# Performance work log

Hardware: AMD Instinct MI355X
Metric: run time of the kernel (lower is better)

Reference implementation:

```python
import jax, jax.numpy as jnp
import numpy as np

N_NODES = 50000
N_EDGES = 1_600_000
IN_FEATS = 256
N_HEADS = 2
OUT_FEATS = 64
NEG_SLOPE = 0.2


def setup_inputs() -> dict:
    key = jax.random.key(0)
    k1, k2, k3, k4, k5, k6 = jax.random.split(key, 6)
    feat = jax.random.normal(k1, (N_NODES, IN_FEATS), dtype=jnp.float32)
    src = jax.random.randint(k2, (N_EDGES,), 0, N_NODES, dtype=jnp.int32)
    dst = jax.random.randint(k3, (N_EDGES,), 0, N_NODES, dtype=jnp.int32)
    W = jax.random.normal(k4, (IN_FEATS, N_HEADS * OUT_FEATS), dtype=jnp.float32) * 0.05
    attn_l = jax.random.normal(k5, (N_HEADS, OUT_FEATS), dtype=jnp.float32) * 0.1
    attn_r = jax.random.normal(k6, (N_HEADS, OUT_FEATS), dtype=jnp.float32) * 0.1
    return {"feat": feat, "src": src, "dst": dst, "W": W, "attn_l": attn_l, "attn_r": attn_r}


def reference(feat, src, dst, W, attn_l, attn_r):
    # node projection: [N, H, F]
    ft = (feat @ W).reshape(N_NODES, N_HEADS, OUT_FEATS)
    el = jnp.einsum('nhf,hf->nh', ft, attn_l)  # [N, H]
    er = jnp.einsum('nhf,hf->nh', ft, attn_r)  # [N, H]
    # per-edge logits + leaky relu
    e = el[src] + er[dst]                      # [E, H]
    e = jnp.where(e > 0, e, NEG_SLOPE * e)
    # segment softmax over incoming edges of each dst node
    m = jax.ops.segment_max(e, dst, num_segments=N_NODES)     # [N, H]
    m = jnp.where(jnp.isfinite(m), m, 0.0)                     # guard empty segments
    e_exp = jnp.exp(e - jax.lax.stop_gradient(m)[dst])         # [E, H]
    s = jax.ops.segment_sum(e_exp, dst, num_segments=N_NODES)  # [N, H]
    a = e_exp / jnp.maximum(s[dst], 1e-20)                     # [E, H]
    # scatter-weighted aggregation: sum_e a_e * ft[src_e] into dst
    msg = ft[src] * a[:, :, None]                              # [E, H, F]
    rst = jax.ops.segment_sum(msg, dst, num_segments=N_NODES)  # [N, H, F]
    return rst
```

## Files before the change

### kernel.cpp

```cpp
#include <hip/hip_runtime.h>
#include <hip/hip_fp16.h>

#define N_NODES 50000
#define N_EDGES 1600000
#define IN_F 256
#define NEG_SLOPE 0.2f
#define CHUNK 1024
#define NCH ((N_NODES + CHUNK - 1) / CHUNK)

__global__ __launch_bounds__(256) void k_gemm(const float* __restrict__ feat,
                                              const float* __restrict__ W,
                                              const float* __restrict__ attn_l,
                                              const float* __restrict__ attn_r,
                                              __half* __restrict__ ft16,
                                              float* __restrict__ el,
                                              float* __restrict__ er) {
  __shared__ __align__(16) float Wl[32 * 128];
  __shared__ __align__(16) float Fl[64 * 33];
  const int tid = threadIdx.x;
  const int cg = tid & 15;
  const int rg = tid >> 4;
  const int col0 = cg * 8, rowt = rg * 4;
  const int row0 = blockIdx.x * 64;
  float acc[4][8];
#pragma unroll
  for (int i = 0; i < 4; ++i)
#pragma unroll
    for (int j = 0; j < 8; ++j) acc[i][j] = 0.f;

  for (int kt = 0; kt < IN_F; kt += 32) {
    __syncthreads();
#pragma unroll
    for (int j = 0; j < 4; ++j) {
      int idx = tid + j * 256;
      ((float4*)Wl)[idx] = ((const float4*)(W + kt * 128))[idx];
    }
#pragma unroll
    for (int j = 0; j < 2; ++j) {
      int r = j * 32 + (tid >> 3);
      int kk = (tid & 7) * 4;
      int grow = row0 + r;
      if (grow >= N_NODES) grow = N_NODES - 1;
      float4 v = *(const float4*)(feat + (size_t)grow * IN_F + kt + kk);
      float* fp = &Fl[r * 33 + kk];
      fp[0] = v.x; fp[1] = v.y; fp[2] = v.z; fp[3] = v.w;
    }
    __syncthreads();
#pragma unroll
    for (int k = 0; k < 32; ++k) {
      float4 w0 = *(const float4*)&Wl[k * 128 + col0];
      float4 w1 = *(const float4*)&Wl[k * 128 + col0 + 4];
#pragma unroll
      for (int i = 0; i < 4; ++i) {
        float f = Fl[(rowt + i) * 33 + k];
        acc[i][0] = fmaf(f, w0.x, acc[i][0]);
        acc[i][1] = fmaf(f, w0.y, acc[i][1]);
        acc[i][2] = fmaf(f, w0.z, acc[i][2]);
        acc[i][3] = fmaf(f, w0.w, acc[i][3]);
        acc[i][4] = fmaf(f, w1.x, acc[i][4]);
        acc[i][5] = fmaf(f, w1.y, acc[i][5]);
        acc[i][6] = fmaf(f, w1.z, acc[i][6]);
        acc[i][7] = fmaf(f, w1.w, acc[i][7]);
      }
    }
  }
  float al[8], ar[8];
#pragma unroll
  for (int j = 0; j < 8; ++j) { al[j] = attn_l[col0 + j]; ar[j] = attn_r[col0 + j]; }
#pragma unroll
  for (int i = 0; i < 4; ++i) {
    int row = row0 + rowt + i;
    float sl = 0.f, sr = 0.f;
#pragma unroll
    for (int j = 0; j < 8; ++j) { sl = fmaf(acc[i][j], al[j], sl); sr = fmaf(acc[i][j], ar[j], sr); }
#pragma unroll
    for (int m = 1; m < 8; m <<= 1) { sl += __shfl_xor(sl, m, 64); sr += __shfl_xor(sr, m, 64); }
    if (row < N_NODES) {
      __half2 h0 = __floats2half2_rn(acc[i][0], acc[i][1]);
      __half2 h1 = __floats2half2_rn(acc[i][2], acc[i][3]);
      __half2 h2 = __floats2half2_rn(acc[i][4], acc[i][5]);
      __half2 h3 = __floats2half2_rn(acc[i][6], acc[i][7]);
      uint4 pk = make_uint4(*(unsigned*)&h0, *(unsigned*)&h1,
                            *(unsigned*)&h2, *(unsigned*)&h3);
      *(uint4*)(ft16 + (size_t)row * 128 + col0) = pk;
      if ((cg & 7) == 0) {
        int h = cg >> 3;
        el[row * 2 + h] = sl;
        er[row * 2 + h] = sr;
      }
    }
  }
}

__global__ __launch_bounds__(256) void k_deg(const int* __restrict__ dst,
                                             int* __restrict__ deg,
                                             ushort* __restrict__ rank) {
  int t = blockIdx.x * 256 + threadIdx.x;
  if (t >= N_EDGES / 4) return;
  int4 d4 = ((const int4*)dst)[t];
  ushort4 r;
  r.x = (ushort)atomicAdd(&deg[d4.x], 1);
  r.y = (ushort)atomicAdd(&deg[d4.y], 1);
  r.z = (ushort)atomicAdd(&deg[d4.z], 1);
  r.w = (ushort)atomicAdd(&deg[d4.w], 1);
  ((ushort4*)rank)[t] = r;
}

__global__ __launch_bounds__(256) void k_scanA(const int* __restrict__ deg,
                                               int* __restrict__ csum) {
  __shared__ int ws[4];
  int b = blockIdx.x, tid = threadIdx.x, lane = tid & 63, w = tid >> 6;
  int i0 = b * CHUNK + tid * 4;
  int s = 0;
#pragma unroll
  for (int j = 0; j < 4; ++j) {
    int i = i0 + j;
    if (i < N_NODES) s += deg[i];
  }
#pragma unroll
  for (int m = 32; m > 0; m >>= 1) s += __shfl_xor(s, m, 64);
  if (lane == 0) ws[w] = s;
  __syncthreads();
  if (tid == 0) csum[b] = ws[0] + ws[1] + ws[2] + ws[3];
}

__global__ void k_scanB(const int* __restrict__ csum, int* __restrict__ coff,
                        int* __restrict__ rowptr) {
  int tid = threadIdx.x;
  int v = (tid < NCH) ? csum[tid] : 0;
  int x = v;
#pragma unroll
  for (int off = 1; off < 64; off <<= 1) {
    int y = __shfl_up(x, off, 64);
    if (tid >= off) x += y;
  }
  if (tid < NCH) coff[tid] = x - v;
  if (tid == NCH - 1) rowptr[N_NODES] = x;
}

__global__ __launch_bounds__(256) void k_scanC(const int* __restrict__ deg,
                                               const int* __restrict__ coff,
                                               int* __restrict__ rowptr) {
  __shared__ int wtot[4];
  int b = blockIdx.x, tid = threadIdx.x, lane = tid & 63, w = tid >> 6;
  int i0 = b * CHUNK + tid * 4;
  int d[4];
#pragma unroll
  for (int j = 0; j < 4; ++j) d[j] = (i0 + j < N_NODES) ? deg[i0 + j] : 0;
  int t1 = d[0] + d[1], t2 = t1 + d[2], t3 = t2 + d[3];
  int x = t3;
#pragma unroll
  for (int off = 1; off < 64; off <<= 1) {
    int y = __shfl_up(x, off, 64);
    if (lane >= off) x += y;
  }
  if (lane == 63) wtot[w] = x;
  __syncthreads();
  int woff = 0;
  for (int j = 0; j < w; ++j) woff += wtot[j];
  int excl = coff[b] + woff + (x - t3);
  int pre[4] = {0, d[0], t1, t2};
#pragma unroll
  for (int j = 0; j < 4; ++j) {
    int i = i0 + j;
    if (i < N_NODES) rowptr[i] = excl + pre[j];
  }
}

__global__ __launch_bounds__(256) void k_sort(const int* __restrict__ src,
                                              const int* __restrict__ dst,
                                              const ushort* __restrict__ rank,
                                              const int* __restrict__ rowptr,
                                              int* __restrict__ srcs) {
  int t = blockIdx.x * 256 + threadIdx.x;
  if (t >= N_EDGES / 4) return;
  int4 s4 = ((const int4*)src)[t];
  int4 d4 = ((const int4*)dst)[t];
  ushort4 r4 = ((const ushort4*)rank)[t];
  srcs[rowptr[d4.x] + r4.x] = s4.x;
  srcs[rowptr[d4.y] + r4.y] = s4.y;
  srcs[rowptr[d4.z] + r4.z] = s4.z;
  srcs[rowptr[d4.w] + r4.w] = s4.w;
}

__global__ __launch_bounds__(256) void k_agg(const int* __restrict__ srcs,
                                             const int* __restrict__ rowptr,
                                             const __half2* __restrict__ ft2,
                                             const float2* __restrict__ el2,
                                             const float2* __restrict__ er2,
                                             float2* __restrict__ out) {
  int t = blockIdx.x * 256 + threadIdx.x;
  int node = t >> 6, lane = t & 63;
  if (node >= N_NODES) return;
  int beg = rowptr[node], end = rowptr[node + 1];
  bool h1 = lane >= 32;
  float2 ern = er2[node];
  float erh = h1 ? ern.y : ern.x;
  float ax = 0.f, ay = 0.f, s = 0.f;
  int i = beg;
  for (; i + 4 <= end; i += 4) {
    int s0 = srcs[i], s1 = srcs[i + 1], s2 = srcs[i + 2], s3 = srcs[i + 3];
    float2 e0 = el2[s0], e1 = el2[s1], e2 = el2[s2], e3 = el2[s3];
    __half2 f0 = ft2[(size_t)s0 * 64 + lane];
    __half2 f1 = ft2[(size_t)s1 * 64 + lane];
    __half2 f2 = ft2[(size_t)s2 * 64 + lane];
    __half2 f3 = ft2[(size_t)s3 * 64 + lane];
    float x0 = (h1 ? e0.y : e0.x) + erh;
    float x1 = (h1 ? e1.y : e1.x) + erh;
    float x2 = (h1 ? e2.y : e2.x) + erh;
    float x3 = (h1 ? e3.y : e3.x) + erh;
    x0 = x0 > 0.f ? x0 : NEG_SLOPE * x0;
    x1 = x1 > 0.f ? x1 : NEG_SLOPE * x1;
    x2 = x2 > 0.f ? x2 : NEG_SLOPE * x2;
    x3 = x3 > 0.f ? x3 : NEG_SLOPE * x3;
    float p0 = __expf(x0), p1 = __expf(x1), p2 = __expf(x2), p3 = __expf(x3);
    float2 g0 = __half22float2(f0);
    float2 g1 = __half22float2(f1);
    float2 g2 = __half22float2(f2);
    float2 g3 = __half22float2(f3);
    ax = fmaf(p0, g0.x, ax); ay = fmaf(p0, g0.y, ay);
    ax = fmaf(p1, g1.x, ax); ay = fmaf(p1, g1.y, ay);
    ax = fmaf(p2, g2.x, ax); ay = fmaf(p2, g2.y, ay);
    ax = fmaf(p3, g3.x, ax); ay = fmaf(p3, g3.y, ay);
    s += (p0 + p1) + (p2 + p3);
  }
  for (; i < end; ++i) {
    int sr = srcs[i];
    float2 e = el2[sr];
    __half2 f = ft2[(size_t)sr * 64 + lane];
    float x = (h1 ? e.y : e.x) + erh;
    x = x > 0.f ? x : NEG_SLOPE * x;
    float p = __expf(x);
    float2 g = __half22float2(f);
    ax = fmaf(p, g.x, ax); ay = fmaf(p, g.y, ay);
    s += p;
  }
  float inv = 1.f / fmaxf(s, 1e-20f);
  out[(size_t)node * 64 + lane] = make_float2(ax * inv, ay * inv);
}

extern "C" void kernel_launch(void* const* d_in, const int* in_sizes, int n_in,
                              void* d_out, int out_size, void* d_ws, size_t ws_size,
                              hipStream_t stream) {
  const float* feat   = (const float*)d_in[0];
  const int*   src    = (const int*)d_in[1];
  const int*   dst    = (const int*)d_in[2];
  const float* W      = (const float*)d_in[3];
  const float* attn_l = (const float*)d_in[4];
  const float* attn_r = (const float*)d_in[5];
  float* out = (float*)d_out;

  char* base = (char*)d_ws;
  size_t off = 0;
  auto bump = [&](size_t bytes) -> void* {
    void* p = base + off;
    off = (off + bytes + 255) & ~(size_t)255;
    return p;
  };
  __half* ft16   = (__half*)bump(sizeof(__half) * N_NODES * 128);
  float*  el     = (float*)bump(sizeof(float) * N_NODES * 2);
  float*  er     = (float*)bump(sizeof(float) * N_NODES * 2);
  int*    deg    = (int*)bump(sizeof(int) * N_NODES);
  int*    csum   = (int*)bump(sizeof(int) * NCH);
  int*    coff   = (int*)bump(sizeof(int) * NCH);
  int*    rowptr = (int*)bump(sizeof(int) * (N_NODES + 1));
  ushort* rank   = (ushort*)bump(sizeof(ushort) * N_EDGES);
  int*    srcs   = (int*)bump(sizeof(int) * N_EDGES);
  (void)ws_size; (void)in_sizes; (void)n_in; (void)out_size;

  (void)hipMemsetAsync(deg, 0, sizeof(int) * N_NODES, stream);

  k_deg<<<(N_EDGES / 4 + 255) / 256, 256, 0, stream>>>(dst, deg, rank);
  k_gemm<<<(N_NODES + 63) / 64, 256, 0, stream>>>(feat, W, attn_l, attn_r, ft16, el, er);
  k_scanA<<<NCH, 256, 0, stream>>>(deg, csum);
  k_scanB<<<1, 64, 0, stream>>>(csum, coff, rowptr);
  k_scanC<<<NCH, 256, 0, stream>>>(deg, coff, rowptr);
  k_sort<<<(N_EDGES / 4 + 255) / 256, 256, 0, stream>>>(src, dst, rank, rowptr, srcs);
  k_agg<<<(N_NODES * 64 + 255) / 256, 256, 0, stream>>>(srcs, rowptr,
      (const __half2*)ft16, (const float2*)el, (const float2*)er, (float2*)out);
}
```

Before: 336.4 us.

## Precompute per-edge attention exponentials during CSR scatter and pack with source index

The scatter kernel now computes leaky-relu and exp of the edge logit for both heads and stores them as a half2 packed with the source index in a 64-bit record. The aggregation kernel reads these records and no longer gathers el per edge or computes exp redundantly in all 64 lanes. Its main loop is unrolled to 8 edges and uses nontemporal loads on the records. The record array doubles in size versus the int source array, and storing unnormalised exp values in fp16 risks overflow or precision loss.

New measurement: 327.1 us. 1.03x faster.

```diff
diff --git a/kernel.cpp b/kernel.cpp
--- a/kernel.cpp
+++ b/kernel.cpp
@@ -167,73 +167,77 @@
   }
 }
 
-__global__ __launch_bounds__(256) void k_sort(const int* __restrict__ src,
-                                              const int* __restrict__ dst,
-                                              const ushort* __restrict__ rank,
-                                              const int* __restrict__ rowptr,
-                                              int* __restrict__ srcs) {
+__device__ __forceinline__ void sort1(int s, int d, int rk,
+                                      const int* __restrict__ rowptr,
+                                      const float2* __restrict__ el2,
+                                      const float2* __restrict__ er2,
+                                      unsigned long long* __restrict__ rec) {
+  float2 a = el2[s];
+  float2 b = er2[d];
+  float e0 = a.x + b.x, e1 = a.y + b.y;
+  e0 = e0 > 0.f ? e0 : NEG_SLOPE * e0;
+  e1 = e1 > 0.f ? e1 : NEG_SLOPE * e1;
+  __half2 h = __floats2half2_rn(__expf(e0), __expf(e1));
+  unsigned long long v =
+      ((unsigned long long)(*(unsigned*)&h) << 32) | (unsigned)s;
+  rec[rowptr[d] + rk] = v;
+}
+
+__global__ __launch_bounds__(256) void k_sortp(const int* __restrict__ src,
+                                               const int* __restrict__ dst,
+                                               const ushort* __restrict__ rank,
+                                               const int* __restrict__ rowptr,
+                                               const float2* __restrict__ el2,
+                                               const float2* __restrict__ er2,
+                                               unsigned long long* __restrict__ rec) {
   int t = blockIdx.x * 256 + threadIdx.x;
   if (t >= N_EDGES / 4) return;
   int4 s4 = ((const int4*)src)[t];
   int4 d4 = ((const int4*)dst)[t];
   ushort4 r4 = ((const ushort4*)rank)[t];
-  srcs[rowptr[d4.x] + r4.x] = s4.x;
-  srcs[rowptr[d4.y] + r4.y] = s4.y;
-  srcs[rowptr[d4.z] + r4.z] = s4.z;
-  srcs[rowptr[d4.w] + r4.w] = s4.w;
-}
-
-__global__ __launch_bounds__(256) void k_agg(const int* __restrict__ srcs,
+  sort1(s4.x, d4.x, r4.x, rowptr, el2, er2, rec);
+  sort1(s4.y, d4.y, r4.y, rowptr, el2, er2, rec);
+  sort1(s4.z, d4.z, r4.z, rowptr, el2, er2, rec);
+  sort1(s4.w, d4.w, r4.w, rowptr, el2, er2, rec);
+}
+
+__global__ __launch_bounds__(256) void k_agg(const unsigned long long* __restrict__ rec,
                                              const int* __restrict__ rowptr,
                                              const __half2* __restrict__ ft2,
-                                             const float2* __restrict__ el2,
-                                             const float2* __restrict__ er2,
                                              float2* __restrict__ out) {
   int t = blockIdx.x * 256 + threadIdx.x;
   int node = t >> 6, lane = t & 63;
   if (node >= N_NODES) return;
   int beg = rowptr[node], end = rowptr[node + 1];
   bool h1 = lane >= 32;
-  float2 ern = er2[node];
-  float erh = h1 ? ern.y : ern.x;
   float ax = 0.f, ay = 0.f, s = 0.f;
   int i = beg;
-  for (; i + 4 <= end; i += 4) {
-    int s0 = srcs[i], s1 = srcs[i + 1], s2 = srcs[i + 2], s3 = srcs[i + 3];
-    float2 e0 = el2[s0], e1 = el2[s1], e2 = el2[s2], e3 = el2[s3];
-    __half2 f0 = ft2[(size_t)s0 * 64 + lane];
-    __half2 f1 = ft2[(size_t)s1 * 64 + lane];
-    __half2 f2 = ft2[(size_t)s2 * 64 + lane];
-    __half2 f3 = ft2[(size_t)s3 * 64 + lane];
-    float x0 = (h1 ? e0.y : e0.x) + erh;
-    float x1 = (h1 ? e1.y : e1.x) + erh;
-    float x2 = (h1 ? e2.y : e2.x) + erh;
-    float x3 = (h1 ? e3.y : e3.x) + erh;
-    x0 = x0 > 0.f ? x0 : NEG_SLOPE * x0;
-    x1 = x1 > 0.f ? x1 : NEG_SLOPE * x1;
-    x2 = x2 > 0.f ? x2 : NEG_SLOPE * x2;
-    x3 = x3 > 0.f ? x3 : NEG_SLOPE * x3;
-    float p0 = __expf(x0), p1 = __expf(x1), p2 = __expf(x2), p3 = __expf(x3);
-    float2 g0 = __half22float2(f0);
-    float2 g1 = __half22float2(f1);
-    float2 g2 = __half22float2(f2);
-    float2 g3 = __half22float2(f3);
-    ax = fmaf(p0, g0.x, ax); ay = fmaf(p0, g0.y, ay);
-    ax = fmaf(p1, g1.x, ax); ay = fmaf(p1, g1.y, ay);
-    ax = fmaf(p2, g2.x, ax); ay = fmaf(p2, g2.y, ay);
-    ax = fmaf(p3, g3.x, ax); ay = fmaf(p3, g3.y, ay);
-    s += (p0 + p1) + (p2 + p3);
+  for (; i + 8 <= end; i += 8) {
+    unsigned long long r[8];
+#pragma unroll
+    for (int j = 0; j < 8; ++j) r[j] = __builtin_nontemporal_load(&rec[i + j]);
+    __half2 f[8];
+#pragma unroll
+    for (int j = 0; j < 8; ++j)
+      f[j] = ft2[(size_t)(unsigned)(r[j] & 0xffffffffu) * 64 + lane];
+#pragma unroll
+    for (int j = 0; j < 8; ++j) {
+      unsigned pw = (unsigned)(r[j] >> 32);
+      float2 p = __half22float2(*(const __half2*)&pw);
+      float a = h1 ? p.y : p.x;
+      float2 g = __half22float2(f[j]);
+      ax = fmaf(a, g.x, ax); ay = fmaf(a, g.y, ay);
+      s += a;
+    }
   }
   for (; i < end; ++i) {
-    int sr = srcs[i];
-    float2 e = el2[sr];
-    __half2 f = ft2[(size_t)sr * 64 + lane];
-    float x = (h1 ? e.y : e.x) + erh;
-    x = x > 0.f ? x : NEG_SLOPE * x;
-    float p = __expf(x);
-    float2 g = __half22float2(f);
-    ax = fmaf(p, g.x, ax); ay = fmaf(p, g.y, ay);
-    s += p;
+    unsigned long long r = rec[i];
+    unsigned pw = (unsigned)(r >> 32);
+    float2 p = __half22float2(*(const __half2*)&pw);
+    float a = h1 ? p.y : p.x;
+    float2 g = __half22float2(ft2[(size_t)(unsigned)(r & 0xffffffffu) * 64 + lane]);
+    ax = fmaf(a, g.x, ax); ay = fmaf(a, g.y, ay);
+    s += a;
   }
   float inv = 1.f / fmaxf(s, 1e-20f);
   out[(size_t)node * 64 + lane] = make_float2(ax * inv, ay * inv);
@@ -265,7 +269,8 @@
   int*    coff   = (int*)bump(sizeof(int) * NCH);
   int*    rowptr = (int*)bump(sizeof(int) * (N_NODES + 1));
   ushort* rank   = (ushort*)bump(sizeof(ushort) * N_EDGES);
-  int*    srcs   = (int*)bump(sizeof(int) * N_EDGES);
+  unsigned long long* rec =
+      (unsigned long long*)bump(sizeof(unsigned long long) * N_EDGES);
   (void)ws_size; (void)in_sizes; (void)n_in; (void)out_size;
 
   (void)hipMemsetAsync(deg, 0, sizeof(int) * N_NODES, stream);
@@ -275,7 +280,8 @@
   k_scanA<<<NCH, 256, 0, stream>>>(deg, csum);
   k_scanB<<<1, 64, 0, stream>>>(csum, coff, rowptr);
   k_scanC<<<NCH, 256, 0, stream>>>(deg, coff, rowptr);
-  k_sort<<<(N_EDGES / 4 + 255) / 256, 256, 0, stream>>>(src, dst, rank, rowptr, srcs);
-  k_agg<<<(N_NODES * 64 + 255) / 256, 256, 0, stream>>>(srcs, rowptr,
-      (const __half2*)ft16, (const float2*)el, (const float2*)er, (float2*)out);
-}
+  k_sortp<<<(N_EDGES / 4 + 255) / 256, 256, 0, stream>>>(src, dst, rank, rowptr,
+      (const float2*)el, (const float2*)er, rec);
+  k_agg<<<(N_NODES * 64 + 255) / 256, 256, 0, stream>>>(rec, rowptr,
+      (const __half2*)ft16, (float2*)out);
+}
```
